# Kernel optimization log

Measured on AMD Instinct MI355X. Metric: run time of the kernel, lower is better.

The kernel has to match this reference:

```python
import jax, jax.numpy as jnp
import numpy as np

T, B, F = 2048, 2, 1024
H = 16
DK = F // H


def setup_inputs() -> dict:
    key = jax.random.key(0)
    ks = jax.random.split(key, 13)
    s = 0.02
    return {
        "query": jax.random.normal(ks[0], (T, B, F), jnp.float32),
        "key": jax.random.normal(ks[1], (T, B, F), jnp.float32),
        "value": jax.random.normal(ks[2], (T, B, F), jnp.float32),
        "key_padding_mask": jax.random.randint(ks[3], (B, T), 0, 2).astype(bool),
        "Wq": jax.random.normal(ks[4], (F, F), jnp.float32) * s,
        "bq": jnp.zeros((F,), jnp.float32),
        "Wk": jax.random.normal(ks[5], (F, F), jnp.float32) * s,
        "bk": jnp.zeros((F,), jnp.float32),
        "Wv": jax.random.normal(ks[6], (F, F), jnp.float32) * s,
        "bv": jnp.zeros((F,), jnp.float32),
        "Wo": jax.random.normal(ks[7], (F, F), jnp.float32) * s,
        "bo": jnp.zeros((F,), jnp.float32),
    }


def reference(query, key, value, key_padding_mask, Wq, bq, Wk, bk, Wv, bv, Wo, bo):
    # inputs are [T, B, F]; module transposes to batch-major [B, T, F]
    q = jnp.swapaxes(query, 0, 1)
    k = jnp.swapaxes(key, 0, 1)
    v = jnp.swapaxes(value, 0, 1)
    nb = q.shape[0]
    # QKV projections, split into heads: [B, H, T, DK]
    def proj(x, W, b):
        y = x @ W.T + b
        return y.reshape(nb, -1, H, DK).transpose(0, 2, 1, 3)
    qh, kh, vh = proj(q, Wq, bq), proj(k, Wk, bk), proj(v, Wv, bv)
    # scores [B, H, Tq, Tk]
    scores = jnp.einsum("bhqd,bhkd->bhqk", qh, kh) / jnp.sqrt(jnp.float32(DK))
    scores = jnp.where(key_padding_mask[:, None, None, :], -jnp.inf, scores)
    attn = jax.nn.softmax(scores, axis=-1)
    # AV + merge heads + out proj (dropout p=0 -> identity)
    ctx = jnp.einsum("bhqk,bhkd->bhqd", attn, vh)
    ctx = ctx.transpose(0, 2, 1, 3).reshape(nb, -1, H * DK)
    out = ctx @ Wo.T + bo
    return jnp.swapaxes(out, 0, 1)  # back to [T, B, F]
```

## Files before the change

kernel.cpp:

```cpp
#include <hip/hip_runtime.h>
#include <hip/hip_bf16.h>
#include <stdint.h>


typedef __bf16 bf16_t;
typedef __bf16 bf16x4 __attribute__((ext_vector_type(4)));
typedef __bf16 bf16x8 __attribute__((ext_vector_type(8)));
typedef float f32x4 __attribute__((ext_vector_type(4)));
typedef unsigned int u32x2 __attribute__((ext_vector_type(2)));

typedef const __attribute__((address_space(1))) void* gas_ptr;
typedef __attribute__((address_space(3))) void* las_ptr;

__device__ __forceinline__ void gload16(const void* g, void* lds) {
    __builtin_amdgcn_global_load_lds((gas_ptr)g, (las_ptr)lds, 16, 0, 0);
}

__device__ __forceinline__ int swz(int o) { return o ^ (((o >> 7) & 7) << 4); }

__device__ __forceinline__ int gofs(int c) {
    return ((c >> 5) << 9) + (((c >> 1) & 3) << 7) + (((c >> 3) & 3) << 5) + ((c & 1) << 4);
}

#define TRREAD(dst, addr, IMM) \
    asm volatile("ds_read_b64_tr_b16 %0, %1 offset:" #IMM : "=v"(dst) : "v"(addr))

#if __has_builtin(__builtin_amdgcn_exp2f)
#define EXP2F(x) __builtin_amdgcn_exp2f(x)
#else
#define EXP2F(x) exp2f(x)
#endif
#if __has_builtin(__builtin_amdgcn_rcpf)
#define RCPF(x) __builtin_amdgcn_rcpf(x)
#else
#define RCPF(x) (1.0f / (x))
#endif

__global__ __launch_bounds__(256) void prep_all_kernel(const float* __restrict__ wq,
                                                       const float* __restrict__ wk,
                                                       const float* __restrict__ wv,
                                                       const float* __restrict__ wo,
                                                       const unsigned char* __restrict__ mraw,
                                                       bf16_t* __restrict__ wdst,
                                                       unsigned long long* __restrict__ mbits) {
    const int bidx = blockIdx.x;
    const int tid = threadIdx.x;
    if (bidx < 2048) {
        int idx = bidx * 256 + tid;
        int which = idx >> 17;
        int loc = idx & 131071;
        const float* src = which == 0 ? wq : which == 1 ? wk : which == 2 ? wv : wo;
        int e0 = loc * 8;
        const float4* s = (const float4*)(src + e0);
        float4 a = s[0], c = s[1];
        bf16x8 o;
        o[0] = (bf16_t)a.x; o[1] = (bf16_t)a.y; o[2] = (bf16_t)a.z; o[3] = (bf16_t)a.w;
        o[4] = (bf16_t)c.x; o[5] = (bf16_t)c.y; o[6] = (bf16_t)c.z; o[7] = (bf16_t)c.w;
        *(bf16x8*)(wdst + (size_t)which * 1048576 + e0) = o;
    } else {
        __shared__ int s_isbyte;
        if (tid == 0) s_isbyte = 0;
        __syncthreads();
        int any = 0;
        for (int i = tid; i < 4096; i += 256)
            if ((i & 3) && mraw[i]) any = 1;
        if (any) atomicOr(&s_isbyte, 1);
        __syncthreads();
        if (tid < 64) {
            int b = tid >> 5, kt = tid & 31;
            unsigned long long bits = 0;
            if (s_isbyte) {
                for (int j = 0; j < 64; ++j)
                    if (mraw[b * 2048 + kt * 64 + j]) bits |= 1ull << j;
            } else {
                const int* ri = (const int*)mraw;
                for (int j = 0; j < 64; ++j)
                    if (ri[b * 2048 + kt * 64 + j]) bits |= 1ull << j;
            }
            mbits[tid] = bits;
        }
    }
}

__global__ __launch_bounds__(256) void gemm_qkv_kernel(const float* __restrict__ x0,
                                                       const float* __restrict__ x1,
                                                       const float* __restrict__ x2,
                                                       const bf16_t* __restrict__ Bw0,
                                                       const float* __restrict__ b0,
                                                       const float* __restrict__ b1,
                                                       const float* __restrict__ b2,
                                                       const unsigned long long* __restrict__ mbits,
                                                       bf16_t* __restrict__ outb) {
    __shared__ __align__(16) bf16_t Asm[128 * 32];
    __shared__ __align__(16) bf16_t Bsm[4][128 * 32];
    const int tid = threadIdx.x;
    const int wave = tid >> 6, lane = tid & 63;
    const int g = lane >> 4, lr = lane & 15;

    const int sid = (blockIdx.x & 7) * 96 + (blockIdx.x >> 3);
    const int z = sid >> 8;
    const int rem = sid & 255;
    const int m0 = (rem >> 3) * 128, n0 = (rem & 7) * 128;

    const float* Xf = z == 0 ? x0 : z == 1 ? x1 : x2;
    const bf16_t* Bw = Bw0 + (size_t)z * 1048576;
    const float* bias = z == 0 ? b0 : z == 1 ? b1 : b2;
    const float qsc = (z == 0) ? 0.18033688f : 1.0f;
    const int wm = (wave >> 1) * 64, wn = (wave & 1) * 64;
    const int srow = wave * 32 + (lane >> 2);
    const int scol = (lane & 3) * 8;

    const int r0 = m0 + srow, r1 = r0 + 16;
    const size_t fb0 = (size_t)((r0 & 2047) * 2 + (r0 >> 11)) * 1024 + scol;
    const size_t fb1 = (size_t)((r1 & 2047) * 2 + (r1 >> 11)) * 1024 + scol;
    const bf16_t* gB0 = Bw + (size_t)(n0 + srow) * 1024 + scol;
    const bf16_t* gB1 = Bw + (size_t)(n0 + srow + 16) * 1024 + scol;
    char* dA0 = (char*)Asm + wave * 2048 + lane * 16;
    char* dA1 = dA0 + 1024;

    f32x4 acc[4][4] = {};
    float4 a00, a01, a10, a11;

    gload16(gB0,      (char*)Bsm[0] + wave * 2048);
    gload16(gB1,      (char*)Bsm[0] + wave * 2048 + 1024);
    a00 = *(const float4*)(Xf + fb0);
    a01 = *(const float4*)(Xf + fb0 + 4);
    a10 = *(const float4*)(Xf + fb1);
    a11 = *(const float4*)(Xf + fb1 + 4);
    gload16(gB0 + 32, (char*)Bsm[1] + wave * 2048);
    gload16(gB1 + 32, (char*)Bsm[1] + wave * 2048 + 1024);

    for (int it = 0; it < 32; ++it) {
        const int k0 = it * 32;
        __builtin_amdgcn_s_barrier();
        __builtin_amdgcn_sched_barrier(0);
        {
            bf16x8 w0, w1;
            w0[0] = (bf16_t)a00.x; w0[1] = (bf16_t)a00.y; w0[2] = (bf16_t)a00.z; w0[3] = (bf16_t)a00.w;
            w0[4] = (bf16_t)a01.x; w0[5] = (bf16_t)a01.y; w0[6] = (bf16_t)a01.z; w0[7] = (bf16_t)a01.w;
            w1[0] = (bf16_t)a10.x; w1[1] = (bf16_t)a10.y; w1[2] = (bf16_t)a10.z; w1[3] = (bf16_t)a10.w;
            w1[4] = (bf16_t)a11.x; w1[5] = (bf16_t)a11.y; w1[6] = (bf16_t)a11.z; w1[7] = (bf16_t)a11.w;
            *(bf16x8*)dA0 = w0;
            *(bf16x8*)dA1 = w1;
        }
        if (it < 31) {
            a00 = *(const float4*)(Xf + fb0 + k0 + 32);
            a01 = *(const float4*)(Xf + fb0 + k0 + 36);
            a10 = *(const float4*)(Xf + fb1 + k0 + 32);
            a11 = *(const float4*)(Xf + fb1 + k0 + 36);
        }
        if (it < 30) {
            gload16(gB0 + k0 + 64, (char*)Bsm[(it + 2) & 3] + wave * 2048);
            gload16(gB1 + k0 + 64, (char*)Bsm[(it + 2) & 3] + wave * 2048 + 1024);
        }
        asm volatile("s_waitcnt lgkmcnt(0)" ::: "memory");
        __builtin_amdgcn_s_barrier();
        __builtin_amdgcn_sched_barrier(0);

        const bf16_t* Bc = Bsm[it & 3];
        bf16x8 af[4], bfr[4];
        #pragma unroll
        for (int mi = 0; mi < 4; ++mi)
            af[mi] = *(const bf16x8*)(Asm + (wm + mi * 16 + lr) * 32 + g * 8);
        #pragma unroll
        for (int ni = 0; ni < 4; ++ni)
            bfr[ni] = *(const bf16x8*)(Bc + (wn + ni * 16 + lr) * 32 + g * 8);
        #pragma unroll
        for (int mi = 0; mi < 4; ++mi)
            #pragma unroll
            for (int ni = 0; ni < 4; ++ni)
                acc[mi][ni] = __builtin_amdgcn_mfma_f32_16x16x32_bf16(af[mi], bfr[ni], acc[mi][ni], 0, 0, 0);
    }

    #pragma unroll
    for (int mi = 0; mi < 4; ++mi) {
        #pragma unroll
        for (int ni = 0; ni < 4; ++ni) {
            int n = n0 + wn + ni * 16 + lr;
            float bs = bias[n];
            #pragma unroll
            for (int i = 0; i < 4; ++i) {
                int m = m0 + wm + mi * 16 + 4 * g + i;
                float v = (acc[mi][ni][i] + bs) * qsc;
                int b = m >> 11, t = m & 2047;
                if (z != 0) {
                    const bool mk = (mbits[b * 32 + (t >> 6)] >> (t & 63)) & 1;
                    if (mk) v = 0.f;
                }
                int hh = n >> 6, dk = n & 63;
                outb[(size_t)z * 4194304 + ((size_t)(b * 16 + hh) * 2048 + t) * 64 + dk] = (bf16_t)v;
            }
        }
    }
}

__global__ __launch_bounds__(256) void gemm_out_kernel(const bf16_t* __restrict__ Ab,
                                                       const bf16_t* __restrict__ Bw,
                                                       const float* __restrict__ bias,
                                                       float* __restrict__ outf) {
    __shared__ __align__(16) bf16_t Asm[128 * 32];
    __shared__ __align__(16) bf16_t Bsm[128 * 32];
    const int tid = threadIdx.x;
    const int wave = tid >> 6, lane = tid & 63;
    const int g = lane >> 4, lr = lane & 15;

    const int sid = (blockIdx.x & 7) * 32 + (blockIdx.x >> 3);
    const int m0 = (sid >> 3) * 128, n0 = (sid & 7) * 128;
    const int wm = (wave >> 1) * 64, wn = (wave & 1) * 64;
    const int srow = wave * 32 + (lane >> 2);
    const int scol = (lane & 3) * 8;
    const int r0 = m0 + srow, r1 = r0 + 16;

    f32x4 acc[4][4] = {};

    for (int k0 = 0; k0 < 1024; k0 += 32) {
        __syncthreads();
        gload16(Ab + (size_t)r0 * 1024 + k0 + scol,               (char*)Asm + wave * 2048);
        gload16(Ab + (size_t)r1 * 1024 + k0 + scol,               (char*)Asm + wave * 2048 + 1024);
        gload16(Bw + (size_t)(n0 + srow) * 1024 + k0 + scol,      (char*)Bsm + wave * 2048);
        gload16(Bw + (size_t)(n0 + srow + 16) * 1024 + k0 + scol, (char*)Bsm + wave * 2048 + 1024);
        __syncthreads();

        bf16x8 af[4], bfr[4];
        #pragma unroll
        for (int mi = 0; mi < 4; ++mi)
            af[mi] = *(const bf16x8*)(Asm + (wm + mi * 16 + lr) * 32 + g * 8);
        #pragma unroll
        for (int ni = 0; ni < 4; ++ni)
            bfr[ni] = *(const bf16x8*)(Bsm + (wn + ni * 16 + lr) * 32 + g * 8);
        #pragma unroll
        for (int mi = 0; mi < 4; ++mi)
            #pragma unroll
            for (int ni = 0; ni < 4; ++ni)
                acc[mi][ni] = __builtin_amdgcn_mfma_f32_16x16x32_bf16(af[mi], bfr[ni], acc[mi][ni], 0, 0, 0);
    }

    #pragma unroll
    for (int mi = 0; mi < 4; ++mi) {
        #pragma unroll
        for (int ni = 0; ni < 4; ++ni) {
            int n = n0 + wn + ni * 16 + lr;
            float bs = bias[n];
            #pragma unroll
            for (int i = 0; i < 4; ++i) {
                int m = m0 + wm + mi * 16 + 4 * g + i;
                int b = m >> 11, t = m & 2047;
                outf[(size_t)t * 2048 + b * 1024 + n] = acc[mi][ni][i] + bs;
            }
        }
    }
}

__global__ __launch_bounds__(256, 2) void attn_kernel(const bf16_t* __restrict__ qh,
                                                      const bf16_t* __restrict__ kh,
                                                      const bf16_t* __restrict__ vh,
                                                      const unsigned long long* __restrict__ mbits,
                                                      bf16_t* __restrict__ ctx) {
    __shared__ __align__(16) bf16_t Ks[2][2][64 * 64];
    __shared__ __align__(16) bf16_t Vs[2][2][64 * 64];

    const int tid = threadIdx.x;
    const int wave = tid >> 6, lane = tid & 63;
    const int g = lane >> 4, lr = lane & 15;
    const int bid = blockIdx.x;
    const int sid = (bid & 7) * 64 + (bid >> 3);
    const int bh = sid >> 4, qc = sid & 15;
    const int b = bh >> 4, h = bh & 15;
    const int q0 = qc * 128;
    const bf16_t* Qg = qh + ((size_t)bh * 2048 + q0) * 64;
    const bf16_t* Kg = kh + (size_t)bh * 2048 * 64;
    const bf16_t* Vg = vh + (size_t)bh * 2048 * 64;
    const unsigned long long* mbp = mbits + b * 32;

    const int dstw = wave * 2048;
    const int dl = dstw + lane * 16;
    const int wq0 = wave * 32;
    const int vs0 = gofs(wave * 128 + lane);
    const int vs1 = gofs(wave * 128 + 64 + lane);

    #pragma unroll
    for (int c = 0; c < 4; ++c)
        gload16((const char*)Qg + swz(wave * 4096 + c * 1024 + lane * 16),
                (char*)Ks[0] + wave * 4096 + c * 1024);
    __syncthreads();
    bf16x8 qf[2][2];
    #pragma unroll
    for (int s = 0; s < 2; ++s) {
        qf[s][0] = *(const bf16x8*)((const char*)Ks[0] + swz((wq0 + s * 16 + lr) * 128 + g * 16));
        qf[s][1] = *(const bf16x8*)((const char*)Ks[0] + swz((wq0 + s * 16 + lr) * 128 + 64 + g * 16));
    }
    __syncthreads();

    #pragma unroll
    for (int u = 0; u < 2; ++u) {
        const char* Kt = (const char*)(Kg + u * 4096);
        const char* Vt = (const char*)(Vg + u * 4096);
        gload16(Kt + swz(dl),        (char*)Ks[0][u] + dstw);
        gload16(Kt + swz(dl + 1024), (char*)Ks[0][u] + dstw + 1024);
        gload16(Vt + vs0,            (char*)Vs[0][u] + dstw);
        gload16(Vt + vs1,            (char*)Vs[0][u] + dstw + 1024);
    }

    bf16x8 ones;
    #pragma unroll
    for (int j = 0; j < 8; ++j) ones[j] = (bf16_t)1.0f;

    f32x4 cacc[2][4] = {};
    f32x4 sacc[2] = {};
    const unsigned vbase = (unsigned)(unsigned long long)(las_ptr)&Vs[0][0][0] + g * 512 + lr * 8;

    for (int m = 0; m < 16; ++m) {
        const int par = m & 1;
        __syncthreads();

        if (m < 15) {
            #pragma unroll
            for (int u = 0; u < 2; ++u) {
                const char* Kn = (const char*)(Kg + (2 * m + 2 + u) * 4096);
                const char* Vn = (const char*)(Vg + (2 * m + 2 + u) * 4096);
                gload16(Kn + swz(dl),        (char*)Ks[par ^ 1][u] + dstw);
                gload16(Kn + swz(dl + 1024), (char*)Ks[par ^ 1][u] + dstw + 1024);
                gload16(Vn + vs0,            (char*)Vs[par ^ 1][u] + dstw);
                gload16(Vn + vs1,            (char*)Vs[par ^ 1][u] + dstw + 1024);
            }
        }

        f32x4 s2[2][2][4];
        __builtin_amdgcn_s_setprio(1);
        #pragma unroll
        for (int u = 0; u < 2; ++u) {
            const char* Kc = (const char*)Ks[par][u];
            #pragma unroll
            for (int st = 0; st < 4; ++st) {
                bf16x8 kf0 = *(const bf16x8*)(Kc + swz((st * 16 + lr) * 128 + g * 16));
                bf16x8 kf1 = *(const bf16x8*)(Kc + swz((st * 16 + lr) * 128 + 64 + g * 16));
                #pragma unroll
                for (int s = 0; s < 2; ++s) {
                    f32x4 zz = {};
                    zz = __builtin_amdgcn_mfma_f32_16x16x32_bf16(kf0, qf[s][0], zz, 0, 0, 0);
                    zz = __builtin_amdgcn_mfma_f32_16x16x32_bf16(kf1, qf[s][1], zz, 0, 0, 0);
                    s2[u][s][st] = zz;
                }
            }
        }
        __builtin_amdgcn_s_setprio(0);

        #pragma unroll
        for (int u = 0; u < 2; ++u) {
            #pragma unroll
            for (int st = 0; st < 4; ++st) {
                #pragma unroll
                for (int i = 0; i < 4; ++i) {
                    s2[u][0][st][i] = EXP2F(s2[u][0][st][i]);
                    s2[u][1][st][i] = EXP2F(s2[u][1][st][i]);
                }
            }
            bf16x8 pb[2][2];
            #pragma unroll
            for (int s = 0; s < 2; ++s)
                #pragma unroll
                for (int kk = 0; kk < 2; ++kk)
                    #pragma unroll
                    for (int j = 0; j < 8; ++j)
                        pb[s][kk][j] = (bf16_t)s2[u][s][2 * kk + (j >> 2)][j & 3];

            const unsigned vb = vbase + (unsigned)par * 16384u + (unsigned)u * 8192u;
            u32x2 t[2][2][4];
            TRREAD(t[0][0][0], vb, 0);    TRREAD(t[0][0][1], vb, 128);
            TRREAD(t[0][0][2], vb, 256);  TRREAD(t[0][0][3], vb, 384);
            TRREAD(t[0][1][0], vb, 2048); TRREAD(t[0][1][1], vb, 2176);
            TRREAD(t[0][1][2], vb, 2304); TRREAD(t[0][1][3], vb, 2432);
            TRREAD(t[1][0][0], vb, 4096); TRREAD(t[1][0][1], vb, 4224);
            TRREAD(t[1][0][2], vb, 4352); TRREAD(t[1][0][3], vb, 4480);
            TRREAD(t[1][1][0], vb, 6144); TRREAD(t[1][1][1], vb, 6272);
            TRREAD(t[1][1][2], vb, 6400); TRREAD(t[1][1][3], vb, 6528);
            asm volatile("s_waitcnt lgkmcnt(0)" ::: "memory");
            __builtin_amdgcn_sched_barrier(0);
            __builtin_amdgcn_s_setprio(1);
            #pragma unroll
            for (int kk = 0; kk < 2; ++kk) {
                sacc[0] = __builtin_amdgcn_mfma_f32_16x16x32_bf16(ones, pb[0][kk], sacc[0], 0, 0, 0);
                sacc[1] = __builtin_amdgcn_mfma_f32_16x16x32_bf16(ones, pb[1][kk], sacc[1], 0, 0, 0);
                #pragma unroll
                for (int ni = 0; ni < 4; ++ni) {
                    union { u32x2 q[2]; bf16x8 v8; } uu;
                    uu.q[0] = t[kk][0][ni];
                    uu.q[1] = t[kk][1][ni];
                    #pragma unroll
                    for (int s = 0; s < 2; ++s)
                        cacc[s][ni] = __builtin_amdgcn_mfma_f32_16x16x32_bf16(uu.v8, pb[s][kk], cacc[s][ni], 0, 0, 0);
                }
            }
            __builtin_amdgcn_s_setprio(0);
        }
    }

    float nm = 0.f;
    #pragma unroll
    for (int i = 0; i < 32; ++i)
        nm += (float)__popcll(mbp[i]);
    #pragma unroll
    for (int s = 0; s < 2; ++s) {
        const float rl = RCPF(sacc[s][0] - nm);
        const int trow = q0 + wq0 + s * 16 + lr;
        #pragma unroll
        for (int ni = 0; ni < 4; ++ni) {
            bf16x4 o;
            #pragma unroll
            for (int i = 0; i < 4; ++i)
                o[i] = (bf16_t)(cacc[s][ni][i] * rl);
            *(bf16x4*)(ctx + ((size_t)b * 2048 + trow) * 1024 + h * 64 + ni * 16 + 4 * g) = o;
        }
    }
}

extern "C" void kernel_launch(void* const* d_in, const int* in_sizes, int n_in,
                              void* d_out, int out_size, void* d_ws, size_t ws_size,
                              hipStream_t stream) {
    const float* query = (const float*)d_in[0];
    const float* key_  = (const float*)d_in[1];
    const float* value = (const float*)d_in[2];
    const unsigned char* kpm_raw = (const unsigned char*)d_in[3];
    const float* Wq = (const float*)d_in[4];
    const float* bq = (const float*)d_in[5];
    const float* Wk = (const float*)d_in[6];
    const float* bk = (const float*)d_in[7];
    const float* Wv = (const float*)d_in[8];
    const float* bv = (const float*)d_in[9];
    const float* Wo = (const float*)d_in[10];
    const float* bo = (const float*)d_in[11];
    float* out = (float*)d_out;

    char* ws = (char*)d_ws;
    size_t off = 0;
    auto alloc = [&](size_t bytes) {
        char* p = ws + off;
        off += (bytes + 255) & ~(size_t)255;
        return p;
    };
    const size_t SZ_X = (size_t)4096 * 1024 * sizeof(bf16_t);
    const size_t SZ_W = (size_t)1024 * 1024 * sizeof(bf16_t);
    bf16_t* wqb = (bf16_t*)alloc(SZ_W);
    bf16_t* wkb = (bf16_t*)alloc(SZ_W);
    bf16_t* wvb = (bf16_t*)alloc(SZ_W);
    bf16_t* wob = (bf16_t*)alloc(SZ_W);
    bf16_t* qhB = (bf16_t*)alloc(SZ_X);
    bf16_t* khB = (bf16_t*)alloc(SZ_X);
    bf16_t* vhB = (bf16_t*)alloc(SZ_X);
    bf16_t* ctxB = (bf16_t*)alloc(SZ_X);
    unsigned long long* mbits = (unsigned long long*)alloc(64 * sizeof(unsigned long long));
    (void)wkb; (void)wvb;

    prep_all_kernel<<<2049, 256, 0, stream>>>(Wq, Wk, Wv, Wo, kpm_raw, wqb, mbits);

    gemm_qkv_kernel<<<768, 256, 0, stream>>>(query, key_, value, wqb,
                                             bq, bk, bv, mbits, qhB);

    attn_kernel<<<512, 256, 0, stream>>>(qhB, khB, vhB, mbits, ctxB);

    gemm_out_kernel<<<256, 256, 0, stream>>>(ctxB, wob, bo, out);
}
```

Before: 122.6 us.

## Widen QKV GEMM K-step to 64 with double-buffered B tiles

Restructures the QKV projection GEMM main loop to process two 32-wide K slices per iteration (16 iterations instead of 32). This halves the number of barrier pairs. The A tile now holds two halves, the B tiles are double-buffered in 64-wide chunks, and prefetch distance becomes one 64-wide step instead of two 32-wide steps. The change reduces synchronization overhead but doubles the fp32 A registers held in flight and shortens B prefetch lookahead in K terms relative to the old 4-buffer ring.

```diff
diff --git a/kernel.cpp b/kernel.cpp
--- a/kernel.cpp
+++ b/kernel.cpp
@@ -91,8 +91,8 @@
                                                        const float* __restrict__ b2,
                                                        const unsigned long long* __restrict__ mbits,
                                                        bf16_t* __restrict__ outb) {
-    __shared__ __align__(16) bf16_t Asm[128 * 32];
-    __shared__ __align__(16) bf16_t Bsm[4][128 * 32];
+    __shared__ __align__(16) bf16_t Asm[2][128 * 32];
+    __shared__ __align__(16) bf16_t Bsm[2][2][128 * 32];
     const int tid = threadIdx.x;
     const int wave = tid >> 6, lane = tid & 63;
     const int g = lane >> 4, lr = lane & 15;
@@ -115,62 +115,84 @@
     const size_t fb1 = (size_t)((r1 & 2047) * 2 + (r1 >> 11)) * 1024 + scol;
     const bf16_t* gB0 = Bw + (size_t)(n0 + srow) * 1024 + scol;
     const bf16_t* gB1 = Bw + (size_t)(n0 + srow + 16) * 1024 + scol;
-    char* dA0 = (char*)Asm + wave * 2048 + lane * 16;
-    char* dA1 = dA0 + 1024;
 
     f32x4 acc[4][4] = {};
-    float4 a00, a01, a10, a11;
-
-    gload16(gB0,      (char*)Bsm[0] + wave * 2048);
-    gload16(gB1,      (char*)Bsm[0] + wave * 2048 + 1024);
-    a00 = *(const float4*)(Xf + fb0);
-    a01 = *(const float4*)(Xf + fb0 + 4);
-    a10 = *(const float4*)(Xf + fb1);
-    a11 = *(const float4*)(Xf + fb1 + 4);
-    gload16(gB0 + 32, (char*)Bsm[1] + wave * 2048);
-    gload16(gB1 + 32, (char*)Bsm[1] + wave * 2048 + 1024);
-
-    for (int it = 0; it < 32; ++it) {
-        const int k0 = it * 32;
+    float4 ar[2][2][2];
+
+#define LOAD_B(it_) do {                                                      \
+        const int kk_ = (it_) * 64;                                           \
+        char* bb_ = (char*)Bsm + (((it_) & 1) * 16384);                       \
+        gload16(gB0 + kk_,      bb_ + wave * 2048);                           \
+        gload16(gB1 + kk_,      bb_ + wave * 2048 + 1024);                    \
+        gload16(gB0 + kk_ + 32, bb_ + 8192 + wave * 2048);                    \
+        gload16(gB1 + kk_ + 32, bb_ + 8192 + wave * 2048 + 1024);             \
+    } while (0)
+
+#define LOAD_A(it_) do {                                                      \
+        const int kk_ = (it_) * 64;                                           \
+        _Pragma("unroll")                                                     \
+        for (int hh_ = 0; hh_ < 2; ++hh_) {                                   \
+            ar[hh_][0][0] = *(const float4*)(Xf + fb0 + kk_ + hh_ * 32);      \
+            ar[hh_][0][1] = *(const float4*)(Xf + fb0 + kk_ + hh_ * 32 + 4);  \
+            ar[hh_][1][0] = *(const float4*)(Xf + fb1 + kk_ + hh_ * 32);      \
+            ar[hh_][1][1] = *(const float4*)(Xf + fb1 + kk_ + hh_ * 32 + 4);  \
+        }                                                                     \
+    } while (0)
+
+    LOAD_B(0);
+    __builtin_amdgcn_sched_barrier(0);
+    LOAD_A(0);
+    __builtin_amdgcn_sched_barrier(0);
+
+    for (int it = 0; it < 16; ++it) {
         __builtin_amdgcn_s_barrier();
         __builtin_amdgcn_sched_barrier(0);
-        {
+        #pragma unroll
+        for (int hh = 0; hh < 2; ++hh) {
             bf16x8 w0, w1;
-            w0[0] = (bf16_t)a00.x; w0[1] = (bf16_t)a00.y; w0[2] = (bf16_t)a00.z; w0[3] = (bf16_t)a00.w;
-            w0[4] = (bf16_t)a01.x; w0[5] = (bf16_t)a01.y; w0[6] = (bf16_t)a01.z; w0[7] = (bf16_t)a01.w;
-            w1[0] = (bf16_t)a10.x; w1[1] = (bf16_t)a10.y; w1[2] = (bf16_t)a10.z; w1[3] = (bf16_t)a10.w;
-            w1[4] = (bf16_t)a11.x; w1[5] = (bf16_t)a11.y; w1[6] = (bf16_t)a11.z; w1[7] = (bf16_t)a11.w;
-            *(bf16x8*)dA0 = w0;
-            *(bf16x8*)dA1 = w1;
-        }
-        if (it < 31) {
-            a00 = *(const float4*)(Xf + fb0 + k0 + 32);
-            a01 = *(const float4*)(Xf + fb0 + k0 + 36);
-            a10 = *(const float4*)(Xf + fb1 + k0 + 32);
-            a11 = *(const float4*)(Xf + fb1 + k0 + 36);
-        }
-        if (it < 30) {
-            gload16(gB0 + k0 + 64, (char*)Bsm[(it + 2) & 3] + wave * 2048);
-            gload16(gB1 + k0 + 64, (char*)Bsm[(it + 2) & 3] + wave * 2048 + 1024);
+            w0[0] = (bf16_t)ar[hh][0][0].x; w0[1] = (bf16_t)ar[hh][0][0].y;
+            w0[2] = (bf16_t)ar[hh][0][0].z; w0[3] = (bf16_t)ar[hh][0][0].w;
+            w0[4] = (bf16_t)ar[hh][0][1].x; w0[5] = (bf16_t)ar[hh][0][1].y;
+            w0[6] = (bf16_t)ar[hh][0][1].z; w0[7] = (bf16_t)ar[hh][0][1].w;
+            w1[0] = (bf16_t)ar[hh][1][0].x; w1[1] = (bf16_t)ar[hh][1][0].y;
+            w1[2] = (bf16_t)ar[hh][1][0].z; w1[3] = (bf16_t)ar[hh][1][0].w;
+            w1[4] = (bf16_t)ar[hh][1][1].x; w1[5] = (bf16_t)ar[hh][1][1].y;
+            w1[6] = (bf16_t)ar[hh][1][1].z; w1[7] = (bf16_t)ar[hh][1][1].w;
+            *(bf16x8*)((char*)Asm + hh * 8192 + wave * 2048 + lane * 16) = w0;
+            *(bf16x8*)((char*)Asm + hh * 8192 + wave * 2048 + 1024 + lane * 16) = w1;
+        }
+        __builtin_amdgcn_sched_barrier(0);
+        if (it < 15) {
+            LOAD_B(it + 1);
+            __builtin_amdgcn_sched_barrier(0);
+            LOAD_A(it + 1);
+            __builtin_amdgcn_sched_barrier(0);
         }
         asm volatile("s_waitcnt lgkmcnt(0)" ::: "memory");
         __builtin_amdgcn_s_barrier();
         __builtin_amdgcn_sched_barrier(0);
 
-        const bf16_t* Bc = Bsm[it & 3];
-        bf16x8 af[4], bfr[4];
-        #pragma unroll
-        for (int mi = 0; mi < 4; ++mi)
-            af[mi] = *(const bf16x8*)(Asm + (wm + mi * 16 + lr) * 32 + g * 8);
-        #pragma unroll
-        for (int ni = 0; ni < 4; ++ni)
-            bfr[ni] = *(const bf16x8*)(Bc + (wn + ni * 16 + lr) * 32 + g * 8);
-        #pragma unroll
-        for (int mi = 0; mi < 4; ++mi)
+        const char* Bc = (const char*)Bsm + (it & 1) * 16384;
+        #pragma unroll
+        for (int hh = 0; hh < 2; ++hh) {
+            bf16x8 af[4], bfr[4];
+            #pragma unroll
+            for (int mi = 0; mi < 4; ++mi)
+                af[mi] = *(const bf16x8*)((const char*)Asm + hh * 8192 +
+                                          ((wm + mi * 16 + lr) * 32 + g * 8) * 2);
             #pragma unroll
             for (int ni = 0; ni < 4; ++ni)
-                acc[mi][ni] = __builtin_amdgcn_mfma_f32_16x16x32_bf16(af[mi], bfr[ni], acc[mi][ni], 0, 0, 0);
-    }
+                bfr[ni] = *(const bf16x8*)(Bc + hh * 8192 +
+                                           ((wn + ni * 16 + lr) * 32 + g * 8) * 2);
+            #pragma unroll
+            for (int mi = 0; mi < 4; ++mi)
+                #pragma unroll
+                for (int ni = 0; ni < 4; ++ni)
+                    acc[mi][ni] = __builtin_amdgcn_mfma_f32_16x16x32_bf16(af[mi], bfr[ni], acc[mi][ni], 0, 0, 0);
+        }
+    }
+#undef LOAD_A
+#undef LOAD_B
 
     #pragma unroll
     for (int mi = 0; mi < 4; ++mi) {
```

Result: slower. 139.3 us (+13.6%).

## Load QKV weight fragments directly from global into registers, bypassing LDS

Applied to the files above, without the earlier changes.

The QKV projection GEMM no longer stages the bf16 weight tile through a 4-deep LDS ring via global_load_lds. Each wave instead loads its own B fragments straight from global memory into registers, double-buffered across a 2x unrolled loop. This cuts LDS footprint and LDS reads, which may raise occupancy. The cost is that the two waves sharing the same wn columns now load the same weight data redundantly. The global loads also sit on the critical path with only one iteration of prefetch.

```diff
diff --git a/kernel.cpp b/kernel.cpp
--- a/kernel.cpp
+++ b/kernel.cpp
@@ -92,7 +92,6 @@
                                                        const unsigned long long* __restrict__ mbits,
                                                        bf16_t* __restrict__ outb) {
     __shared__ __align__(16) bf16_t Asm[128 * 32];
-    __shared__ __align__(16) bf16_t Bsm[4][128 * 32];
     const int tid = threadIdx.x;
     const int wave = tid >> 6, lane = tid & 63;
     const int g = lane >> 4, lr = lane & 15;
@@ -113,64 +112,71 @@
     const int r0 = m0 + srow, r1 = r0 + 16;
     const size_t fb0 = (size_t)((r0 & 2047) * 2 + (r0 >> 11)) * 1024 + scol;
     const size_t fb1 = (size_t)((r1 & 2047) * 2 + (r1 >> 11)) * 1024 + scol;
-    const bf16_t* gB0 = Bw + (size_t)(n0 + srow) * 1024 + scol;
-    const bf16_t* gB1 = Bw + (size_t)(n0 + srow + 16) * 1024 + scol;
+    const bf16_t* gBf0 = Bw + (size_t)(n0 + wn + 0  + lr) * 1024 + g * 8;
+    const bf16_t* gBf1 = Bw + (size_t)(n0 + wn + 16 + lr) * 1024 + g * 8;
+    const bf16_t* gBf2 = Bw + (size_t)(n0 + wn + 32 + lr) * 1024 + g * 8;
+    const bf16_t* gBf3 = Bw + (size_t)(n0 + wn + 48 + lr) * 1024 + g * 8;
     char* dA0 = (char*)Asm + wave * 2048 + lane * 16;
     char* dA1 = dA0 + 1024;
 
     f32x4 acc[4][4] = {};
     float4 a00, a01, a10, a11;
-
-    gload16(gB0,      (char*)Bsm[0] + wave * 2048);
-    gload16(gB1,      (char*)Bsm[0] + wave * 2048 + 1024);
+    bf16x8 bA[4], bB[4];
+
     a00 = *(const float4*)(Xf + fb0);
     a01 = *(const float4*)(Xf + fb0 + 4);
     a10 = *(const float4*)(Xf + fb1);
     a11 = *(const float4*)(Xf + fb1 + 4);
-    gload16(gB0 + 32, (char*)Bsm[1] + wave * 2048);
-    gload16(gB1 + 32, (char*)Bsm[1] + wave * 2048 + 1024);
-
-    for (int it = 0; it < 32; ++it) {
-        const int k0 = it * 32;
-        __builtin_amdgcn_s_barrier();
-        __builtin_amdgcn_sched_barrier(0);
-        {
-            bf16x8 w0, w1;
-            w0[0] = (bf16_t)a00.x; w0[1] = (bf16_t)a00.y; w0[2] = (bf16_t)a00.z; w0[3] = (bf16_t)a00.w;
-            w0[4] = (bf16_t)a01.x; w0[5] = (bf16_t)a01.y; w0[6] = (bf16_t)a01.z; w0[7] = (bf16_t)a01.w;
-            w1[0] = (bf16_t)a10.x; w1[1] = (bf16_t)a10.y; w1[2] = (bf16_t)a10.z; w1[3] = (bf16_t)a10.w;
-            w1[4] = (bf16_t)a11.x; w1[5] = (bf16_t)a11.y; w1[6] = (bf16_t)a11.z; w1[7] = (bf16_t)a11.w;
-            *(bf16x8*)dA0 = w0;
-            *(bf16x8*)dA1 = w1;
-        }
-        if (it < 31) {
-            a00 = *(const float4*)(Xf + fb0 + k0 + 32);
-            a01 = *(const float4*)(Xf + fb0 + k0 + 36);
-            a10 = *(const float4*)(Xf + fb1 + k0 + 32);
-            a11 = *(const float4*)(Xf + fb1 + k0 + 36);
-        }
-        if (it < 30) {
-            gload16(gB0 + k0 + 64, (char*)Bsm[(it + 2) & 3] + wave * 2048);
-            gload16(gB1 + k0 + 64, (char*)Bsm[(it + 2) & 3] + wave * 2048 + 1024);
-        }
-        asm volatile("s_waitcnt lgkmcnt(0)" ::: "memory");
-        __builtin_amdgcn_s_barrier();
-        __builtin_amdgcn_sched_barrier(0);
-
-        const bf16_t* Bc = Bsm[it & 3];
-        bf16x8 af[4], bfr[4];
-        #pragma unroll
-        for (int mi = 0; mi < 4; ++mi)
-            af[mi] = *(const bf16x8*)(Asm + (wm + mi * 16 + lr) * 32 + g * 8);
-        #pragma unroll
-        for (int ni = 0; ni < 4; ++ni)
-            bfr[ni] = *(const bf16x8*)(Bc + (wn + ni * 16 + lr) * 32 + g * 8);
-        #pragma unroll
-        for (int mi = 0; mi < 4; ++mi)
-            #pragma unroll
-            for (int ni = 0; ni < 4; ++ni)
-                acc[mi][ni] = __builtin_amdgcn_mfma_f32_16x16x32_bf16(af[mi], bfr[ni], acc[mi][ni], 0, 0, 0);
-    }
+    bA[0] = *(const bf16x8*)(gBf0);
+    bA[1] = *(const bf16x8*)(gBf1);
+    bA[2] = *(const bf16x8*)(gBf2);
+    bA[3] = *(const bf16x8*)(gBf3);
+
+#define QKV_BODY(it_, CUR, NXT) do {                                          \
+        const int k0_ = (it_) * 32;                                           \
+        __builtin_amdgcn_s_barrier();         \
+        __builtin_amdgcn_sched_barrier(0);                                    \
+        {     \
+            bf16x8 w0, w1;                                                    \
+            w0[0] = (bf16_t)a00.x; w0[1] = (bf16_t)a00.y; w0[2] = (bf16_t)a00.z; w0[3] = (bf16_t)a00.w; \
+            w0[4] = (bf16_t)a01.x; w0[5] = (bf16_t)a01.y; w0[6] = (bf16_t)a01.z; w0[7] = (bf16_t)a01.w; \
+            w1[0] = (bf16_t)a10.x; w1[1] = (bf16_t)a10.y; w1[2] = (bf16_t)a10.z; w1[3] = (bf16_t)a10.w; \
+            w1[4] = (bf16_t)a11.x; w1[5] = (bf16_t)a11.y; w1[6] = (bf16_t)a11.z; w1[7] = (bf16_t)a11.w; \
+            *(bf16x8*)dA0 = w0;                                               \
+            *(bf16x8*)dA1 = w1;                                               \
+        }                                                                     \
+        if ((it_) < 31) {                                                     \
+              \
+            a00 = *(const float4*)(Xf + fb0 + k0_ + 32);                      \
+            a01 = *(const float4*)(Xf + fb0 + k0_ + 36);                      \
+            a10 = *(const float4*)(Xf + fb1 + k0_ + 32);                      \
+            a11 = *(const float4*)(Xf + fb1 + k0_ + 36);                      \
+            NXT[0] = *(const bf16x8*)(gBf0 + k0_ + 32);                       \
+            NXT[1] = *(const bf16x8*)(gBf1 + k0_ + 32);                       \
+            NXT[2] = *(const bf16x8*)(gBf2 + k0_ + 32);                       \
+            NXT[3] = *(const bf16x8*)(gBf3 + k0_ + 32);                       \
+        }                                                                     \
+        asm volatile("s_waitcnt lgkmcnt(0)" ::: "memory");    \
+        __builtin_amdgcn_s_barrier();                \
+        __builtin_amdgcn_sched_barrier(0);                                    \
+        {                                                                     \
+            bf16x8 af[4];                                                     \
+            _Pragma("unroll")                                                 \
+            for (int mi = 0; mi < 4; ++mi)                                    \
+                af[mi] = *(const bf16x8*)(Asm + (wm + mi * 16 + lr) * 32 + g * 8); \
+            _Pragma("unroll")                                                 \
+            for (int mi = 0; mi < 4; ++mi)                                    \
+                _Pragma("unroll")                                             \
+                for (int ni = 0; ni < 4; ++ni)                                \
+                    acc[mi][ni] = __builtin_amdgcn_mfma_f32_16x16x32_bf16(af[mi], CUR[ni], acc[mi][ni], 0, 0, 0); \
+        }                                                                     \
+    } while (0)
+
+    for (int it = 0; it < 32; it += 2) {
+        QKV_BODY(it,     bA, bB);
+        QKV_BODY(it + 1, bB, bA);
+    }
+#undef QKV_BODY
 
     #pragma unroll
     for (int mi = 0; mi < 4; ++mi) {
```

New measurement: 156.7 us. 1.28x slower.
